# Kernel optimization log

Measured on AMD Instinct MI355X. Metric: run time of the kernel, lower is better.

The kernel has to match this reference:

```python
import jax, jax.numpy as jnp
import numpy as np

B, S, IN_DIM, MEM, LAYERS, HEADS, TOP_K = 64, 256, 512, 256, 3, 8, 200


def setup_inputs() -> dict:
    key = jax.random.key(0)
    ks = jax.random.split(key, 16)
    inputs = jax.random.normal(ks[0], (B, S, IN_DIM), jnp.float32)
    # dependency-style sparse 0/1 adjacency, symmetric with self loops
    a = (jax.random.uniform(ks[1], (B, S, S)) < 0.05).astype(jnp.float32)
    adj = jnp.clip(a + jnp.swapaxes(a, -1, -2) + jnp.eye(S, dtype=jnp.float32), 0.0, 1.0)
    lengths = jnp.maximum(jax.random.randint(ks[2], (B,), 0, S + 1), 32)
    pad = jnp.arange(S)[None, :] >= lengths[:, None]  # [B,S] True at pad positions
    score_mask = pad[:, None, :, None] | pad[:, None, None, :]  # [B,1,S,S]
    d = {"adj": adj, "inputs": inputs, "score_mask": score_mask}

    def lin(k, din, dout):
        k1, k2 = jax.random.split(k)
        s = 1.0 / np.sqrt(din)
        return (jax.random.uniform(k1, (din, dout), jnp.float32, -s, s),
                jax.random.uniform(k2, (dout,), jnp.float32, -s, s))

    ki = 3
    for l in range(LAYERS):
        w, b = lin(ks[ki], IN_DIM + l * MEM, MEM); ki += 1
        d[f"W{l}_w"], d[f"W{l}_b"] = w, b
    for i in range(LAYERS - 1):
        din = IN_DIM + (i + 1) * MEM
        qw, qb = lin(ks[ki], din, din); ki += 1
        kw, kb = lin(ks[ki], din, din); ki += 1
        d[f"attn{i}_qw"], d[f"attn{i}_qb"] = qw, qb
        d[f"attn{i}_kw"], d[f"attn{i}_kb"] = kw, kb
    return d


def _gcn_layer(adj, x, denom, W, b):
    # AxW = W(adj @ x) / denom ; out = relu(AxW) + W(x)   (dropout=identity, eval)
    AxW = ((adj @ x) @ W + b) / denom
    return jax.nn.relu(AxW) + (x @ W + b)


def _mha_adj(x, qw, qb, kw, kb, mask):
    Bn, Sn, D = x.shape
    dk = D // HEADS
    q = (x @ qw + qb).reshape(Bn, Sn, HEADS, dk).transpose(0, 2, 1, 3)
    k = (x @ kw + kb).reshape(Bn, Sn, HEADS, dk).transpose(0, 2, 1, 3)
    scores = jnp.einsum('bhqd,bhkd->bhqk', q, k) / jnp.sqrt(jnp.float32(dk))
    scores = jnp.where(mask, jnp.float32(-1e9), scores)
    keep = (~mask[:, :, :, 0:1]).astype(scores.dtype)  # zero out pad query rows
    return jax.nn.softmax(scores, axis=-1) * keep


def _select(m, top_num):
    # per-batch top-k threshold over flattened [S*S], symmetrize, diag := 1
    Bn, Sn, _ = m.shape
    flat = m.reshape(Bn, -1)
    thr = jax.lax.top_k(flat, top_num)[0][:, -1:]
    sel = (flat >= thr).astype(m.dtype).reshape(Bn, Sn, Sn)
    sel = sel + jnp.swapaxes(sel, -1, -2)
    eye = jnp.eye(Sn, dtype=m.dtype)
    return sel * (1.0 - eye) + eye


def reference(adj, inputs, score_mask, W0_w, W0_b, W1_w, W1_b, W2_w, W2_b,
              attn0_qw, attn0_qb, attn0_kw, attn0_kb,
              attn1_qw, attn1_qb, attn1_kw, attn1_kb):
    Ws = [(W0_w, W0_b), (W1_w, W1_b), (W2_w, W2_b)]
    attns = [(attn0_qw, attn0_qb, attn0_kw, attn0_kb),
             (attn1_qw, attn1_qb, attn1_kw, attn1_kb)]
    denom = adj.sum(2, keepdims=True) + 1.0
    out = _gcn_layer(adj, inputs, denom, *Ws[0])
    x = inputs
    for i in range(1, LAYERS):
        x = jnp.concatenate([x, out], axis=-1)  # growing concatenated features
        a = _mha_adj(x, *attns[i - 1], score_mask)  # [B,H,S,S]
        a = a.sum(axis=1)  # second_layer='sum' branch
        a = _select(a, TOP_K) * a
        denom = a.sum(2, keepdims=True) + 1.0
        out = _gcn_layer(a, x, denom, *Ws[i])
    return out
```

## Files before the change

### kernel.cpp

```cpp
#include <hip/hip_runtime.h>
#include <math.h>


typedef __attribute__((ext_vector_type(8))) short s16x8;
typedef __attribute__((ext_vector_type(4))) short s16x4;
typedef __attribute__((ext_vector_type(4))) float f32x4;

__device__ __forceinline__ short f2bf(float x) {
    unsigned u = __float_as_uint(x);
    u += 0x7FFF + ((u >> 16) & 1);
    return (short)(u >> 16);
}
__device__ __forceinline__ float bf2f(short h) {
    return __uint_as_float(((unsigned)(unsigned short)h) << 16);
}

__device__ __forceinline__ void gl2l(const void* g, void* l) {
    __builtin_amdgcn_global_load_lds(
        (const __attribute__((address_space(1))) unsigned int*)g,
        (__attribute__((address_space(3))) unsigned int*)l, 16, 0, 0);
}

__device__ __forceinline__ float blk_sum(float v, float* sb) {
#pragma unroll
    for (int o = 32; o; o >>= 1) v += __shfl_down(v, o);
    int lane = threadIdx.x & 63, w = threadIdx.x >> 6;
    if (!lane) sb[w] = v;
    __syncthreads();
    float r = sb[0] + sb[1] + sb[2] + sb[3];
    __syncthreads();
    return r;
}

__global__ void init_flags(int* flags) {
    if (threadIdx.x < 3) flags[threadIdx.x] = 0;
}

__global__ void detect_mask(const unsigned int* __restrict__ w, int nwords, int* flags) {
    int stride = gridDim.x * blockDim.x;
    int l_u8 = 0, l_f32 = 0, l_nz = 0;
    for (int i = blockIdx.x * blockDim.x + threadIdx.x; i < nwords; i += stride) {
        unsigned v = w[i];
        if (v) {
            l_nz = 1;
            if (v == 0x3F800000u) l_f32 = 1;
            else if (v > 1u) l_u8 = 1;
        }
    }
    if (__ballot(l_u8) && (threadIdx.x & 63) == 0) atomicOr(&flags[0], 1);
    if (__ballot(l_f32) && (threadIdx.x & 63) == 0) atomicOr(&flags[1], 1);
    if (__ballot(l_nz) && (threadIdx.x & 63) == 0) atomicOr(&flags[2], 1);
}

__global__ void extract_pad(const void* __restrict__ mask, const int* __restrict__ flags,
                            unsigned char* __restrict__ pad) {
    int b = blockIdx.x, i = threadIdx.x;
    int v;
    size_t idx = (size_t)b * 65536 + (size_t)i * 256;
    if (flags[0]) v = ((const unsigned char*)mask)[idx] != 0;
    else if (flags[2]) v = ((const unsigned int*)mask)[idx] != 0;
    else v = 0;
    pad[b * 256 + i] = (unsigned char)v;
}

__global__ void rowsum_plus1(const float* __restrict__ x, float* __restrict__ out) {
    __shared__ float sb[4];
    int row = blockIdx.x;
    float v = x[(size_t)row * 256 + threadIdx.x];
    float r = blk_sum(v, sb);
    if (!threadIdx.x) out[row] = r + 1.f;
}

__global__ void split_mat(const float* __restrict__ src, int ldsrc, int width,
                          short* __restrict__ dh, short* __restrict__ dl, int ldd) {
    int row = blockIdx.x;
    for (int c = threadIdx.x; c < width; c += 256) {
        float v = src[(size_t)row * ldsrc + c];
        short h = f2bf(v);
        dh[(size_t)row * ldd + c] = h;
        dl[(size_t)row * ldd + c] = f2bf(v - bf2f(h));
    }
}

__global__ void transpose_split(const float* __restrict__ in,
                                short* __restrict__ outh, short* __restrict__ outl,
                                int R, int C, int HR, long PSTR, int rowoff, int outld) {
    __shared__ float tile[32][33];
    int c0 = blockIdx.x * 32, r0 = blockIdx.y * 32;
    int tx = threadIdx.x & 31, ty = threadIdx.x >> 5;
    for (int rr = ty; rr < 32; rr += 8)
        tile[rr][tx] = in[(size_t)(r0 + rr) * C + c0 + tx];
    __syncthreads();
    for (int rr = ty; rr < 32; rr += 8) {
        float v = tile[tx][rr];
        int orow = c0 + rr;
        size_t o = (size_t)(orow / HR) * PSTR + (size_t)((orow % HR) + rowoff) * outld + (r0 + tx);
        short h = f2bf(v);
        outh[o] = h;
        outl[o] = f2bf(v - bf2f(h));
    }
}

__global__ void pack_bias2(const float* __restrict__ qb, const float* __restrict__ kb,
                           float* __restrict__ dst, int D) {
    int i = blockIdx.x * 256 + threadIdx.x;
    if (i < D) {
        int p = i / (D / 2), r = i % (D / 2);
        dst[(size_t)p * D + r] = qb[i];
        dst[(size_t)p * D + D / 2 + r] = kb[i];
    }
}

__global__ __launch_bounds__(256) void mgemm(
    const short* __restrict__ Ah, const short* __restrict__ Al,
    const short* __restrict__ Bh, const short* __restrict__ Bl,
    const float* __restrict__ bias,
    float* __restrict__ C, short* __restrict__ Ch, short* __restrict__ Cl,
    short* __restrict__ CTh, short* __restrict__ CTl,
    const float* __restrict__ denom, const unsigned char* __restrict__ padArr,
    int K, int lda, int ldb, int ldc, int coloff, int zdiv,
    long sA1, long sA2, long sB1, long sB2, long sC1, long sC2,
    long sCT, long sD, float alpha, int mode, int skipmode, int swap) {
    int z = blockIdx.z, zq = z / zdiv, zr = z % zdiv;
    int m0, n0;
    if (swap) { m0 = blockIdx.x * 128; n0 = blockIdx.y * 128; }
    else      { m0 = blockIdx.y * 128; n0 = blockIdx.x * 128; }
    if (skipmode == 1 && padArr[m0]) return;
    if (skipmode == 2 && (padArr[zr * 256 + m0] || padArr[zr * 256 + n0])) return;
    const short* Ahb = Ah + (size_t)zq * sA1 + (size_t)zr * sA2;
    const short* Alb = Al + (size_t)zq * sA1 + (size_t)zr * sA2;
    const short* Bhb = Bh + (size_t)zq * sB1 + (size_t)zr * sB2;
    const short* Blb = Bl + (size_t)zq * sB1 + (size_t)zr * sB2;
    size_t offC = (size_t)zq * sC1 + (size_t)zr * sC2;
    __shared__ short lds[16384];
    int t = threadIdx.x;
    int lane = t & 63, w = t >> 6;
    int wm = w >> 1, wn = w & 1;
    f32x4 acc[4][4];
#pragma unroll
    for (int i = 0; i < 4; ++i)
#pragma unroll
        for (int j = 0; j < 4; ++j)
            acc[i][j] = (f32x4){0.f, 0.f, 0.f, 0.f};

    for (int k0 = 0; k0 < K; k0 += 32) {
        __syncthreads();
#pragma unroll
        for (int p = 0; p < 2; ++p) {
            int s = t + p * 256;
            int mi = (s >> 6) * 16 + (s & 15);
            int koff = k0 + ((s >> 4) & 3) * 8;
            size_t oa = (size_t)(m0 + mi) * lda + koff;
            size_t ob = (size_t)(n0 + mi) * ldb + koff;
            gl2l(Ahb + oa, &lds[s * 8]);
            gl2l(Alb + oa, &lds[4096 + s * 8]);
            gl2l(Bhb + ob, &lds[8192 + s * 8]);
            gl2l(Blb + ob, &lds[12288 + s * 8]);
        }
        __syncthreads();
        s16x8 ah[4], al4[4], bh[4], bl4[4];
#pragma unroll
        for (int i = 0; i < 4; ++i) {
            int off = ((wm * 4 + i) * 64 + lane) * 8;
            ah[i] = *(const s16x8*)&lds[off];
            al4[i] = *(const s16x8*)&lds[4096 + off];
        }
#pragma unroll
        for (int j = 0; j < 4; ++j) {
            int off = ((wn * 4 + j) * 64 + lane) * 8;
            bh[j] = *(const s16x8*)&lds[8192 + off];
            bl4[j] = *(const s16x8*)&lds[12288 + off];
        }
#pragma unroll
        for (int i = 0; i < 4; ++i)
#pragma unroll
            for (int j = 0; j < 4; ++j) {
                acc[i][j] = __builtin_amdgcn_mfma_f32_16x16x32_bf16(ah[i], bh[j], acc[i][j], 0, 0, 0);
                acc[i][j] = __builtin_amdgcn_mfma_f32_16x16x32_bf16(ah[i], bl4[j], acc[i][j], 0, 0, 0);
                acc[i][j] = __builtin_amdgcn_mfma_f32_16x16x32_bf16(al4[i], bh[j], acc[i][j], 0, 0, 0);
            }
    }

    int col = lane & 15, quad = lane >> 4;
#pragma unroll
    for (int i = 0; i < 4; ++i)
#pragma unroll
        for (int j = 0; j < 4; ++j) {
            int mg = m0 + wm * 64 + i * 16 + quad * 4;
            int ng = n0 + wn * 64 + j * 16 + col;
            f32x4 v = acc[i][j];
            if (mode == 0) {
                float bz = bias ? bias[ng] : 0.f;
                float o[4];
#pragma unroll
                for (int r = 0; r < 4; ++r) o[r] = v[r] * alpha + bz;
                if (C) {
                    float* Cb = C + offC;
#pragma unroll
                    for (int r = 0; r < 4; ++r)
                        Cb[(size_t)(mg + r) * ldc + coloff + ng] = o[r];
                }
                if (Ch) {
                    short* Chb = Ch + offC;
                    short* Clb = Cl + offC;
#pragma unroll
                    for (int r = 0; r < 4; ++r) {
                        short hh = f2bf(o[r]);
                        Chb[(size_t)(mg + r) * ldc + coloff + ng] = hh;
                        Clb[(size_t)(mg + r) * ldc + coloff + ng] = f2bf(o[r] - bf2f(hh));
                    }
                }
                if (CTh) {
                    size_t cb = (size_t)zr * sCT + (size_t)(mg >> 8) * 65536 + (size_t)ng * 256 + (mg & 255);
                    s16x4 hv, lv;
#pragma unroll
                    for (int r = 0; r < 4; ++r) {
                        short hh = f2bf(o[r]);
                        hv[r] = hh;
                        lv[r] = f2bf(o[r] - bf2f(hh));
                    }
                    *(s16x4*)&CTh[cb] = hv;
                    *(s16x4*)&CTl[cb] = lv;
                }
            } else {
                float bz = bias[ng];
                size_t cb = (size_t)zr * sCT + (size_t)(mg >> 8) * 65536 + (size_t)ng * 256 + (mg & 255);
                s16x4 th = *(const s16x4*)&CTh[cb];
                s16x4 tl = *(const s16x4*)&CTl[cb];
                const float* Db = denom + (size_t)zr * sD;
#pragma unroll
                for (int r = 0; r < 4; ++r) {
                    float sk = bf2f(th[r]) + bf2f(tl[r]);
                    float u = (v[r] + bz) / Db[mg + r];
                    float o = fmaxf(u, 0.f) + sk + bz;
                    if (C) {
                        C[offC + (size_t)(mg + r) * ldc + coloff + ng] = o;
                    } else {
                        short hh = f2bf(o);
                        Ch[offC + (size_t)(mg + r) * ldc + coloff + ng] = hh;
                        Cl[offC + (size_t)(mg + r) * ldc + coloff + ng] = f2bf(o - bf2f(hh));
                    }
                }
            }
        }
}

__global__ void softmax_headsum2(const float* __restrict__ scores,
                                 const unsigned char* __restrict__ pad,
                                 float* __restrict__ a, int accum) {
    int row = blockIdx.x * 4 + (threadIdx.x >> 6);
    int lane = threadIdx.x & 63;
    int b = row >> 8;
    float* arow = a + (size_t)row * 256;
    if (pad[row]) {
        if (!accum) ((float4*)arow)[lane] = make_float4(0.f, 0.f, 0.f, 0.f);
        return;
    }
    unsigned pw = *(const unsigned*)(pad + (b << 8) + lane * 4);
    float4 racc;
    if (accum) racc = ((float4*)arow)[lane];
    else racc = make_float4(0.f, 0.f, 0.f, 0.f);
#pragma unroll
    for (int hh = 0; hh < 2; ++hh) {
        float4 s = ((const float4*)(scores + (size_t)hh * 4194304 + (size_t)row * 256))[lane];
        if (pw & 0x000000FFu) s.x = -1e9f;
        if (pw & 0x0000FF00u) s.y = -1e9f;
        if (pw & 0x00FF0000u) s.z = -1e9f;
        if (pw & 0xFF000000u) s.w = -1e9f;
        float m = fmaxf(fmaxf(s.x, s.y), fmaxf(s.z, s.w));
#pragma unroll
        for (int o = 32; o; o >>= 1) m = fmaxf(m, __shfl_xor(m, o));
        float e0 = expf(s.x - m), e1 = expf(s.y - m), e2 = expf(s.z - m), e3 = expf(s.w - m);
        float sum = e0 + e1 + e2 + e3;
#pragma unroll
        for (int o = 32; o; o >>= 1) sum += __shfl_xor(sum, o);
        float inv = 1.f / sum;
        racc.x += e0 * inv; racc.y += e1 * inv; racc.z += e2 * inv; racc.w += e3 * inv;
    }
    ((float4*)arow)[lane] = racc;
}

__global__ void tk_init(unsigned* ghist, unsigned* prefix, int* krem) {
    int i = blockIdx.x * 256 + threadIdx.x;
    ghist[i] = 0;
    if (i < 64) { prefix[i] = 0; krem[i] = 200; }
}

__global__ void tk_hist(const float* __restrict__ a, const unsigned* __restrict__ prefix,
                        unsigned* __restrict__ ghist, int shift) {
    __shared__ unsigned h[256];
    int b = blockIdx.x >> 4, slice = blockIdx.x & 15;
    h[threadIdx.x] = 0;
    __syncthreads();
    unsigned pfx = prefix[b];
    const unsigned* ab = (const unsigned*)(a + (size_t)b * 65536) + slice * 4096;
    for (int i = threadIdx.x; i < 4096; i += 256) {
        unsigned u = ab[i];
        if ((shift == 24) || ((u >> (shift + 8)) == pfx)) atomicAdd(&h[(u >> shift) & 255], 1u);
    }
    __syncthreads();
    if (h[threadIdx.x]) atomicAdd(&ghist[b * 256 + threadIdx.x], h[threadIdx.x]);
}

__global__ void tk_pick(unsigned* __restrict__ ghist, unsigned* __restrict__ prefix,
                        int* __restrict__ krem, float* __restrict__ thr, int last) {
    __shared__ unsigned h[256];
    int b = blockIdx.x;
    h[threadIdx.x] = ghist[b * 256 + threadIdx.x];
    ghist[b * 256 + threadIdx.x] = 0;
    __syncthreads();
    if (!threadIdx.x) {
        int k = krem[b];
        unsigned c = 0;
        int bin = 255;
        for (; bin >= 0; --bin) { c += h[bin]; if ((int)c >= k) break; }
        if (bin < 0) bin = 0;
        krem[b] = k - (int)(c - h[bin]);
        unsigned p = (prefix[b] << 8) | (unsigned)bin;
        prefix[b] = p;
        if (last) thr[b] = __uint_as_float(p);
    }
}

__global__ void select_apply(const float* __restrict__ a, const float* __restrict__ thr,
                             short* __restrict__ a2h, short* __restrict__ a2l,
                             float* __restrict__ denom) {
    __shared__ float sb[4];
    int row = blockIdx.x;
    int b = row >> 8, i = row & 255, j = threadIdx.x;
    const float* ab = a + (size_t)b * 65536;
    float tb = thr[b];
    float v = ab[i * 256 + j];
    float vt = ab[j * 256 + i];
    float sel = (v >= tb ? 1.f : 0.f) + (vt >= tb ? 1.f : 0.f);
    if (i == j) sel = 1.f;
    float av = v * sel;
    short hh = f2bf(av);
    a2h[(size_t)row * 256 + j] = hh;
    a2l[(size_t)row * 256 + j] = f2bf(av - bf2f(hh));
    float r = blk_sum(av, sb);
    if (!j) denom[row] = r + 1.f;
}

extern "C" void kernel_launch(void* const* d_in, const int* in_sizes, int n_in,
                              void* d_out, int out_size, void* d_ws, size_t ws_size,
                              hipStream_t stream) {
    const float* adj = (const float*)d_in[0];
    const float* x0 = (const float*)d_in[1];
    const void* mask = d_in[2];
    const float* Wls[3] = {(const float*)d_in[3], (const float*)d_in[5], (const float*)d_in[7]};
    const float* bls[3] = {(const float*)d_in[4], (const float*)d_in[6], (const float*)d_in[8]};
    const float* qws[2] = {(const float*)d_in[9], (const float*)d_in[13]};
    const float* qbs[2] = {(const float*)d_in[10], (const float*)d_in[14]};
    const float* kws[2] = {(const float*)d_in[11], (const float*)d_in[15]};
    const float* kbs[2] = {(const float*)d_in[12], (const float*)d_in[16]};

    char* base = (char*)d_ws;
    size_t cur = 0;
    auto alloc = [&](size_t bytes) -> void* {
        cur = (cur + 1023) & ~(size_t)1023;
        void* p = base + cur;
        cur += bytes;
        return p;
    };
    const size_t NROW = 16384;
    int* flags = (int*)alloc(12);
    unsigned char* pad = (unsigned char*)alloc(NROW);
    float* denom = (float*)alloc(NROW * 4);
    float* thr = (float*)alloc(256);
    unsigned* prefix = (unsigned*)alloc(256);
    int* krem = (int*)alloc(256);
    unsigned* ghist = (unsigned*)alloc(64 * 256 * 4);
    short* WTh = (short*)alloc((size_t)2304 * 256 * 2);
    short* WTl = (short*)alloc((size_t)2304 * 256 * 2);
    short* qkwPh = (short*)alloc((size_t)2 * 1024 * 1024 * 2);
    short* qkwPl = (short*)alloc((size_t)2 * 1024 * 1024 * 2);
    float* qkb = (float*)alloc((size_t)2 * 1024 * 4);
    short* xh = (short*)alloc(NROW * 1024 * 2);
    short* xl = (short*)alloc(NROW * 1024 * 2);
    char* Sreg = (char*)alloc((size_t)2 * 64 * 65536 * 4);
    float* a = (float*)alloc(NROW * 256 * 4);
    short* a2h = (short*)alloc(NROW * 256 * 2);
    short* a2l = (short*)alloc(NROW * 256 * 2);
    short* QKh = (short*)alloc(NROW * 1024 * 2);
    short* QKl = (short*)alloc(NROW * 1024 * 2);
    if (ws_size < cur) return;

    short* tzTh = (short*)Sreg;
    short* tzTl = (short*)Sreg + (size_t)64 * 65536;
    float* scores = (float*)Sreg;
    short* adjh = QKh;
    short* adjl = QKl;
    const int Ks[3] = {512, 768, 1024};
    const long offW[3] = {0, (long)512 * 256, (long)(512 + 768) * 256};

    init_flags<<<1, 64, 0, stream>>>(flags);
    detect_mask<<<64, 256, 0, stream>>>((const unsigned int*)mask, 1048576, flags);
    extract_pad<<<64, 256, 0, stream>>>(mask, flags, pad);
    rowsum_plus1<<<16384, 256, 0, stream>>>(adj, denom);
    split_mat<<<16384, 256, 0, stream>>>(x0, 512, 512, xh, xl, 1024);
    split_mat<<<16384, 256, 0, stream>>>(adj, 256, 256, adjh, adjl, 256);
    for (int l = 0; l < 3; ++l)
        transpose_split<<<dim3(8, Ks[l] / 32), 256, 0, stream>>>(
            Wls[l], WTh + offW[l], WTl + offW[l], Ks[l], 256, 256, 0, 0, Ks[l]);

    for (int l = 0; l < 3; ++l) {
        int Kl = Ks[l];
        mgemm<<<dim3(128, 2, 1), 256, 0, stream>>>(
            xh, xl, WTh + offW[l], WTl + offW[l], nullptr,
            nullptr, nullptr, nullptr, tzTh, tzTl, nullptr, nullptr,
            Kl, 1024, Kl, 0, 0, 1,
            0, 0, 0, 0, 0, 0, 0, 0, 1.f, 0, 0, 1);
        const short* Aah = (l == 0) ? adjh : a2h;
        const short* Aal = (l == 0) ? adjl : a2l;
        if (l < 2) {
            mgemm<<<dim3(2, 2, 64), 256, 0, stream>>>(
                Aah, Aal, tzTh, tzTl, bls[l],
                nullptr, xh, xl, tzTh, tzTl, denom, nullptr,
                256, 256, 256, 1024, Kl, 64,
                0, 65536, 0, 65536, 0, (long)256 * 1024, 65536, 256, 1.f, 1, 0, 0);
        } else {
            mgemm<<<dim3(2, 2, 64), 256, 0, stream>>>(
                Aah, Aal, tzTh, tzTl, bls[l],
                (float*)d_out, nullptr, nullptr, tzTh, tzTl, denom, nullptr,
                256, 256, 256, 256, 0, 64,
                0, 65536, 0, 65536, 0, 65536, 65536, 256, 1.f, 1, 0, 0);
            break;
        }

        int D = Ks[l + 1], dk = D / 8, HD = D / 2;
        float scale = 1.f / sqrtf((float)dk);
        transpose_split<<<dim3(D / 32, D / 32), 256, 0, stream>>>(
            qws[l], qkwPh, qkwPl, D, D, HD, (long)D * D, 0, D);
        transpose_split<<<dim3(D / 32, D / 32), 256, 0, stream>>>(
            kws[l], qkwPh, qkwPl, D, D, HD, (long)D * D, HD, D);
        pack_bias2<<<4, 256, 0, stream>>>(qbs[l], kbs[l], qkb, D);

        for (int p = 0; p < 2; ++p) {
            mgemm<<<dim3(128, D / 128, 1), 256, 0, stream>>>(
                xh, xl, qkwPh + (size_t)p * D * D, qkwPl + (size_t)p * D * D, qkb + (size_t)p * D,
                nullptr, QKh, QKl, nullptr, nullptr, nullptr, pad,
                D, 1024, D, D, 0, 1,
                0, 0, 0, 0, 0, 0, 0, 0, 1.f, 0, 1, 1);
            for (int hp = 0; hp < 2; ++hp) {
                mgemm<<<dim3(2, 2, 128), 256, 0, stream>>>(
                    QKh + (size_t)(hp * 2) * dk, QKl + (size_t)(hp * 2) * dk,
                    QKh + HD + (size_t)(hp * 2) * dk, QKl + HD + (size_t)(hp * 2) * dk,
                    nullptr, scores, nullptr, nullptr, nullptr, nullptr, nullptr, pad,
                    dk, D, D, 256, 0, 64,
                    dk, (long)256 * D, dk, (long)256 * D, (long)64 * 65536, 65536,
                    0, 0, scale, 0, 2, 0);
                softmax_headsum2<<<4096, 256, 0, stream>>>(scores, pad, a, (p * 2 + hp) ? 1 : 0);
            }
        }
        tk_init<<<64, 256, 0, stream>>>(ghist, prefix, krem);
        for (int pp = 0; pp < 4; ++pp) {
            tk_hist<<<1024, 256, 0, stream>>>(a, prefix, ghist, 24 - 8 * pp);
            tk_pick<<<64, 256, 0, stream>>>(ghist, prefix, krem, thr, pp == 3);
        }
        select_apply<<<16384, 256, 0, stream>>>(a, thr, a2h, a2l, denom);
    }
}
```

Measured before the change: 1.358 ms.

## Replace dense adjacency GEMM with sparsity-skipping SpMM and compact live-tile list

The adj@(xW) aggregation now runs in a new fp32 SpMM-style kernel. It skips zero adjacency entries, computes the row-sum denominator inline, and fuses the relu/skip epilogue. This replaces the split-bf16 dense MFMA GEMM and drops the separate rowsum and adjacency-split kernels. The Q/K projection GEMM now launches over a compacted list of live (non-pad) row tiles instead of early-exiting blocks. The trade-off is per-element branches and scalar fp32 FMAs in place of matrix cores, which pays off only while the adjacency stays very sparse.

```diff
diff --git a/kernel.cpp b/kernel.cpp
--- a/kernel.cpp
+++ b/kernel.cpp
@@ -3,7 +3,6 @@
 
 
 typedef __attribute__((ext_vector_type(8))) short s16x8;
-typedef __attribute__((ext_vector_type(4))) short s16x4;
 typedef __attribute__((ext_vector_type(4))) float f32x4;
 
 __device__ __forceinline__ short f2bf(float x) {
@@ -19,17 +18,6 @@
     __builtin_amdgcn_global_load_lds(
         (const __attribute__((address_space(1))) unsigned int*)g,
         (__attribute__((address_space(3))) unsigned int*)l, 16, 0, 0);
-}
-
-__device__ __forceinline__ float blk_sum(float v, float* sb) {
-#pragma unroll
-    for (int o = 32; o; o >>= 1) v += __shfl_down(v, o);
-    int lane = threadIdx.x & 63, w = threadIdx.x >> 6;
-    if (!lane) sb[w] = v;
-    __syncthreads();
-    float r = sb[0] + sb[1] + sb[2] + sb[3];
-    __syncthreads();
-    return r;
 }
 
 __global__ void init_flags(int* flags) {
@@ -63,12 +51,13 @@
     pad[b * 256 + i] = (unsigned char)v;
 }
 
-__global__ void rowsum_plus1(const float* __restrict__ x, float* __restrict__ out) {
-    __shared__ float sb[4];
-    int row = blockIdx.x;
-    float v = x[(size_t)row * 256 + threadIdx.x];
-    float r = blk_sum(v, sb);
-    if (!threadIdx.x) out[row] = r + 1.f;
+__global__ void build_live(const unsigned char* __restrict__ pad, int* __restrict__ live) {
+    if (threadIdx.x == 0) {
+        int c = 0;
+        for (int t = 0; t < 128; ++t)
+            if (!pad[t * 128]) live[1 + c++] = t;
+        live[0] = c;
+    }
 }
 
 __global__ void split_mat(const float* __restrict__ src, int ldsrc, int width,
@@ -116,17 +105,20 @@
     const short* __restrict__ Bh, const short* __restrict__ Bl,
     const float* __restrict__ bias,
     float* __restrict__ C, short* __restrict__ Ch, short* __restrict__ Cl,
-    short* __restrict__ CTh, short* __restrict__ CTl,
-    const float* __restrict__ denom, const unsigned char* __restrict__ padArr,
+    const unsigned char* __restrict__ padArr, const int* __restrict__ liveArr,
     int K, int lda, int ldb, int ldc, int coloff, int zdiv,
     long sA1, long sA2, long sB1, long sB2, long sC1, long sC2,
-    long sCT, long sD, float alpha, int mode, int skipmode, int swap) {
+    float alpha, int skipmode, int swap) {
     int z = blockIdx.z, zq = z / zdiv, zr = z % zdiv;
     int m0, n0;
     if (swap) { m0 = blockIdx.x * 128; n0 = blockIdx.y * 128; }
     else      { m0 = blockIdx.y * 128; n0 = blockIdx.x * 128; }
-    if (skipmode == 1 && padArr[m0]) return;
     if (skipmode == 2 && (padArr[zr * 256 + m0] || padArr[zr * 256 + n0])) return;
+    if (skipmode == 3) {
+        int cnt = liveArr[0];
+        if ((int)blockIdx.x >= cnt) return;
+        m0 = liveArr[1 + blockIdx.x] * 128;
+    }
     const short* Ahb = Ah + (size_t)zq * sA1 + (size_t)zr * sA2;
     const short* Alb = Al + (size_t)zq * sA1 + (size_t)zr * sA2;
     const short* Bhb = Bh + (size_t)zq * sB1 + (size_t)zr * sB2;
@@ -189,60 +181,83 @@
             int mg = m0 + wm * 64 + i * 16 + quad * 4;
             int ng = n0 + wn * 64 + j * 16 + col;
             f32x4 v = acc[i][j];
-            if (mode == 0) {
-                float bz = bias ? bias[ng] : 0.f;
-                float o[4];
-#pragma unroll
-                for (int r = 0; r < 4; ++r) o[r] = v[r] * alpha + bz;
-                if (C) {
-                    float* Cb = C + offC;
-#pragma unroll
-                    for (int r = 0; r < 4; ++r)
-                        Cb[(size_t)(mg + r) * ldc + coloff + ng] = o[r];
-                }
-                if (Ch) {
-                    short* Chb = Ch + offC;
-                    short* Clb = Cl + offC;
-#pragma unroll
-                    for (int r = 0; r < 4; ++r) {
-                        short hh = f2bf(o[r]);
-                        Chb[(size_t)(mg + r) * ldc + coloff + ng] = hh;
-                        Clb[(size_t)(mg + r) * ldc + coloff + ng] = f2bf(o[r] - bf2f(hh));
-                    }
-                }
-                if (CTh) {
-                    size_t cb = (size_t)zr * sCT + (size_t)(mg >> 8) * 65536 + (size_t)ng * 256 + (mg & 255);
-                    s16x4 hv, lv;
-#pragma unroll
-                    for (int r = 0; r < 4; ++r) {
-                        short hh = f2bf(o[r]);
-                        hv[r] = hh;
-                        lv[r] = f2bf(o[r] - bf2f(hh));
-                    }
-                    *(s16x4*)&CTh[cb] = hv;
-                    *(s16x4*)&CTl[cb] = lv;
-                }
-            } else {
-                float bz = bias[ng];
-                size_t cb = (size_t)zr * sCT + (size_t)(mg >> 8) * 65536 + (size_t)ng * 256 + (mg & 255);
-                s16x4 th = *(const s16x4*)&CTh[cb];
-                s16x4 tl = *(const s16x4*)&CTl[cb];
-                const float* Db = denom + (size_t)zr * sD;
+            float bz = bias ? bias[ng] : 0.f;
+            float o[4];
+#pragma unroll
+            for (int r = 0; r < 4; ++r) o[r] = v[r] * alpha + bz;
+            if (C) {
+                float* Cb = C + offC;
+#pragma unroll
+                for (int r = 0; r < 4; ++r)
+                    Cb[(size_t)(mg + r) * ldc + coloff + ng] = o[r];
+            }
+            if (Ch) {
+                short* Chb = Ch + offC;
+                short* Clb = Cl + offC;
 #pragma unroll
                 for (int r = 0; r < 4; ++r) {
-                    float sk = bf2f(th[r]) + bf2f(tl[r]);
-                    float u = (v[r] + bz) / Db[mg + r];
-                    float o = fmaxf(u, 0.f) + sk + bz;
-                    if (C) {
-                        C[offC + (size_t)(mg + r) * ldc + coloff + ng] = o;
-                    } else {
-                        short hh = f2bf(o);
-                        Ch[offC + (size_t)(mg + r) * ldc + coloff + ng] = hh;
-                        Cl[offC + (size_t)(mg + r) * ldc + coloff + ng] = f2bf(o - bf2f(hh));
-                    }
+                    short hh = f2bf(o[r]);
+                    Chb[(size_t)(mg + r) * ldc + coloff + ng] = hh;
+                    Clb[(size_t)(mg + r) * ldc + coloff + ng] = f2bf(o[r] - bf2f(hh));
                 }
             }
         }
+}
+
+__global__ void spmm_gcn(const float* __restrict__ A, const float* __restrict__ tz,
+                         const float* __restrict__ bias,
+                         short* __restrict__ oh, short* __restrict__ ol,
+                         float* __restrict__ of, int ldo, int coloff) {
+    int row = blockIdx.x * 4 + (threadIdx.x >> 6);
+    int lane = threadIdx.x & 63;
+    int b = row >> 8;
+    float4 av = ((const float4*)(A + (size_t)row * 256))[lane];
+    const float* tzb = tz + (size_t)(b << 8) * 256;
+    float4 acc = make_float4(0.f, 0.f, 0.f, 0.f);
+    float rs = av.x + av.y + av.z + av.w;
+#pragma unroll
+    for (int o = 32; o; o >>= 1) rs += __shfl_xor(rs, o);
+    for (int s = 0; s < 64; ++s) {
+        float vx = __shfl(av.x, s), vy = __shfl(av.y, s);
+        float vz = __shfl(av.z, s), vw = __shfl(av.w, s);
+        const float* tj = tzb + (size_t)(s << 2) * 256;
+        if (vx != 0.f) {
+            float4 tv = ((const float4*)tj)[lane];
+            acc.x += vx * tv.x; acc.y += vx * tv.y; acc.z += vx * tv.z; acc.w += vx * tv.w;
+        }
+        if (vy != 0.f) {
+            float4 tv = ((const float4*)(tj + 256))[lane];
+            acc.x += vy * tv.x; acc.y += vy * tv.y; acc.z += vy * tv.z; acc.w += vy * tv.w;
+        }
+        if (vz != 0.f) {
+            float4 tv = ((const float4*)(tj + 512))[lane];
+            acc.x += vz * tv.x; acc.y += vz * tv.y; acc.z += vz * tv.z; acc.w += vz * tv.w;
+        }
+        if (vw != 0.f) {
+            float4 tv = ((const float4*)(tj + 768))[lane];
+            acc.x += vw * tv.x; acc.y += vw * tv.y; acc.z += vw * tv.z; acc.w += vw * tv.w;
+        }
+    }
+    float inv = 1.f / (rs + 1.f);
+    float4 b4 = ((const float4*)bias)[lane];
+    float4 t4 = ((const float4*)(tz + (size_t)row * 256))[lane];
+    float4 o;
+    o.x = fmaxf((acc.x + b4.x) * inv, 0.f) + t4.x + b4.x;
+    o.y = fmaxf((acc.y + b4.y) * inv, 0.f) + t4.y + b4.y;
+    o.z = fmaxf((acc.z + b4.z) * inv, 0.f) + t4.z + b4.z;
+    o.w = fmaxf((acc.w + b4.w) * inv, 0.f) + t4.w + b4.w;
+    if (of) {
+        ((float4*)(of + (size_t)row * ldo))[lane] = o;
+    } else {
+        size_t base = (size_t)row * ldo + coloff + lane * 4;
+        float vv[4] = {o.x, o.y, o.z, o.w};
+#pragma unroll
+        for (int r = 0; r < 4; ++r) {
+            short hh = f2bf(vv[r]);
+            oh[base + r] = hh;
+            ol[base + r] = f2bf(vv[r] - bf2f(hh));
+        }
+    }
 }
 
 __global__ void softmax_headsum2(const float* __restrict__ scores,
@@ -323,9 +338,7 @@
 }
 
 __global__ void select_apply(const float* __restrict__ a, const float* __restrict__ thr,
-                             short* __restrict__ a2h, short* __restrict__ a2l,
-                             float* __restrict__ denom) {
-    __shared__ float sb[4];
+                             float* __restrict__ a2) {
     int row = blockIdx.x;
     int b = row >> 8, i = row & 255, j = threadIdx.x;
     const float* ab = a + (size_t)b * 65536;
@@ -334,12 +347,7 @@
     float vt = ab[j * 256 + i];
     float sel = (v >= tb ? 1.f : 0.f) + (vt >= tb ? 1.f : 0.f);
     if (i == j) sel = 1.f;
-    float av = v * sel;
-    short hh = f2bf(av);
-    a2h[(size_t)row * 256 + j] = hh;
-    a2l[(size_t)row * 256 + j] = f2bf(av - bf2f(hh));
-    float r = blk_sum(av, sb);
-    if (!j) denom[row] = r + 1.f;
+    a2[(size_t)row * 256 + j] = v * sel;
 }
 
 extern "C" void kernel_launch(void* const* d_in, const int* in_sizes, int n_in,
@@ -366,10 +374,10 @@
     const size_t NROW = 16384;
     int* flags = (int*)alloc(12);
     unsigned char* pad = (unsigned char*)alloc(NROW);
-    float* denom = (float*)alloc(NROW * 4);
     float* thr = (float*)alloc(256);
     unsigned* prefix = (unsigned*)alloc(256);
     int* krem = (int*)alloc(256);
+    int* live = (int*)alloc(516);
     unsigned* ghist = (unsigned*)alloc(64 * 256 * 4);
     short* WTh = (short*)alloc((size_t)2304 * 256 * 2);
     short* WTl = (short*)alloc((size_t)2304 * 256 * 2);
@@ -378,28 +386,22 @@
     float* qkb = (float*)alloc((size_t)2 * 1024 * 4);
     short* xh = (short*)alloc(NROW * 1024 * 2);
     short* xl = (short*)alloc(NROW * 1024 * 2);
-    char* Sreg = (char*)alloc((size_t)2 * 64 * 65536 * 4);
+    float* tzf = (float*)alloc(NROW * 256 * 4);
+    float* scores = (float*)alloc((size_t)2 * 64 * 65536 * 4);
     float* a = (float*)alloc(NROW * 256 * 4);
-    short* a2h = (short*)alloc(NROW * 256 * 2);
-    short* a2l = (short*)alloc(NROW * 256 * 2);
+    float* a2f = (float*)alloc(NROW * 256 * 4);
     short* QKh = (short*)alloc(NROW * 1024 * 2);
     short* QKl = (short*)alloc(NROW * 1024 * 2);
     if (ws_size < cur) return;
 
-    short* tzTh = (short*)Sreg;
-    short* tzTl = (short*)Sreg + (size_t)64 * 65536;
-    float* scores = (float*)Sreg;
-    short* adjh = QKh;
-    short* adjl = QKl;
     const int Ks[3] = {512, 768, 1024};
     const long offW[3] = {0, (long)512 * 256, (long)(512 + 768) * 256};
 
     init_flags<<<1, 64, 0, stream>>>(flags);
     detect_mask<<<64, 256, 0, stream>>>((const unsigned int*)mask, 1048576, flags);
     extract_pad<<<64, 256, 0, stream>>>(mask, flags, pad);
-    rowsum_plus1<<<16384, 256, 0, stream>>>(adj, denom);
+    build_live<<<1, 64, 0, stream>>>(pad, live);
     split_mat<<<16384, 256, 0, stream>>>(x0, 512, 512, xh, xl, 1024);
-    split_mat<<<16384, 256, 0, stream>>>(adj, 256, 256, adjh, adjl, 256);
     for (int l = 0; l < 3; ++l)
         transpose_split<<<dim3(8, Ks[l] / 32), 256, 0, stream>>>(
             Wls[l], WTh + offW[l], WTl + offW[l], Ks[l], 256, 256, 0, 0, Ks[l]);
@@ -408,23 +410,16 @@
         int Kl = Ks[l];
         mgemm<<<dim3(128, 2, 1), 256, 0, stream>>>(
             xh, xl, WTh + offW[l], WTl + offW[l], nullptr,
-            nullptr, nullptr, nullptr, tzTh, tzTl, nullptr, nullptr,
-            Kl, 1024, Kl, 0, 0, 1,
-            0, 0, 0, 0, 0, 0, 0, 0, 1.f, 0, 0, 1);
-        const short* Aah = (l == 0) ? adjh : a2h;
-        const short* Aal = (l == 0) ? adjl : a2l;
+            tzf, nullptr, nullptr, nullptr, nullptr,
+            Kl, 1024, Kl, 256, 0, 1,
+            0, 0, 0, 0, 0, 0, 1.f, 0, 1);
+        const float* Aadj = (l == 0) ? adj : a2f;
         if (l < 2) {
-            mgemm<<<dim3(2, 2, 64), 256, 0, stream>>>(
-                Aah, Aal, tzTh, tzTl, bls[l],
-                nullptr, xh, xl, tzTh, tzTl, denom, nullptr,
-                256, 256, 256, 1024, Kl, 64,
-                0, 65536, 0, 65536, 0, (long)256 * 1024, 65536, 256, 1.f, 1, 0, 0);
+            spmm_gcn<<<4096, 256, 0, stream>>>(
+                Aadj, tzf, bls[l], xh, xl, nullptr, 1024, Kl);
         } else {
-            mgemm<<<dim3(2, 2, 64), 256, 0, stream>>>(
-                Aah, Aal, tzTh, tzTl, bls[l],
-                (float*)d_out, nullptr, nullptr, tzTh, tzTl, denom, nullptr,
-                256, 256, 256, 256, 0, 64,
-                0, 65536, 0, 65536, 0, 65536, 65536, 256, 1.f, 1, 0, 0);
+            spmm_gcn<<<4096, 256, 0, stream>>>(
+                Aadj, tzf, bls[l], nullptr, nullptr, (float*)d_out, 256, 0);
             break;
         }
 
@@ -439,17 +434,17 @@
         for (int p = 0; p < 2; ++p) {
             mgemm<<<dim3(128, D / 128, 1), 256, 0, stream>>>(
                 xh, xl, qkwPh + (size_t)p * D * D, qkwPl + (size_t)p * D * D, qkb + (size_t)p * D,
-                nullptr, QKh, QKl, nullptr, nullptr, nullptr, pad,
+                nullptr, QKh, QKl, nullptr, live,
                 D, 1024, D, D, 0, 1,
-                0, 0, 0, 0, 0, 0, 0, 0, 1.f, 0, 1, 1);
+                0, 0, 0, 0, 0, 0, 1.f, 3, 1);
             for (int hp = 0; hp < 2; ++hp) {
                 mgemm<<<dim3(2, 2, 128), 256, 0, stream>>>(
                     QKh + (size_t)(hp * 2) * dk, QKl + (size_t)(hp * 2) * dk,
                     QKh + HD + (size_t)(hp * 2) * dk, QKl + HD + (size_t)(hp * 2) * dk,
-                    nullptr, scores, nullptr, nullptr, nullptr, nullptr, nullptr, pad,
+                    nullptr, scores, nullptr, nullptr, pad, nullptr,
                     dk, D, D, 256, 0, 64,
                     dk, (long)256 * D, dk, (long)256 * D, (long)64 * 65536, 65536,
-                    0, 0, scale, 0, 2, 0);
+                    scale, 2, 0);
                 softmax_headsum2<<<4096, 256, 0, stream>>>(scores, pad, a, (p * 2 + hp) ? 1 : 0);
             }
         }
@@ -458,6 +453,6 @@
             tk_hist<<<1024, 256, 0, stream>>>(a, prefix, ghist, 24 - 8 * pp);
             tk_pick<<<64, 256, 0, stream>>>(ghist, prefix, krem, thr, pp == 3);
         }
-        select_apply<<<16384, 256, 0, stream>>>(a, thr, a2h, a2l, denom);
-    }
-}
+        select_apply<<<16384, 256, 0, stream>>>(a, thr, a2f);
+    }
+}
```

New measurement: 1.469 ms. 1.08x slower.
